# Kernel optimization log

Hardware: AMD Instinct MI355X
Metric: run time of the kernel (lower is better)

## Reference

```python
import jax, jax.numpy as jnp
import numpy as np

B, D, L = 16384, 2048, 6

def setup_inputs() -> dict:
    key = jax.random.key(0)
    kx, kw = jax.random.split(key)
    x = jax.random.normal(kx, (B, D), dtype=jnp.float32)
    # cross weights: xavier_normal on (D,1) -> std = sqrt(2/(D+1)); stacked [L, D]
    std = float(np.sqrt(2.0 / (D + 1)))
    W = jax.random.normal(kw, (L, D), dtype=jnp.float32) * std
    b = jnp.zeros((L, D), dtype=jnp.float32)  # bias params init to zeros
    return {"x": x, "W": W, "b": b}

def reference(x, W, b):
    # Original per layer: x_l = (x0 @ x_l^T) @ w_i + b_i + x_l
    # Algebraically identical: x_l = x0 * (x_l . w_i) + b_i + x_l  (scalar per row)
    x_l = x
    for i in range(W.shape[0]):
        s = jnp.einsum('bd,d->b', x_l, W[i])          # [B]
        x_l = x * s[:, None] + b[i][None, :] + x_l     # [B, D]
    return x_l
```

## Files before the change

kernel.cpp:

```cpp
#include <hip/hip_runtime.h>

#define B_ROWS   16384
#define D_DIM    2048
#define L_LAYERS 6

#define ROW_THREADS 256
#define ROW_WAVES   (ROW_THREADS / 64)
#define ROW_BLOCKS  (B_ROWS / ROW_WAVES)
#define PRE_THREADS 1024
#define WS_FLOATS   (D_DIM + L_LAYERS)

typedef float f32x4 __attribute__((ext_vector_type(4)));


__global__ __launch_bounds__(PRE_THREADS) void precompute_Ue(
    const float* __restrict__ W,
    const float* __restrict__ b,
    float* __restrict__ ws)
{
    __shared__ float red[PRE_THREADS / 64][L_LAYERS];
    const int t    = threadIdx.x;
    const int lane = t & 63;
    const int wid  = t >> 6;
    const int base = t * 2;

    float2 prefix = make_float2(0.f, 0.f);
    float e_red[L_LAYERS];
    #pragma unroll
    for (int l = 0; l < L_LAYERS; ++l) {
        const float2 wv = *(const float2*)(W + l * D_DIM + base);
        const float2 bv = *(const float2*)(b + l * D_DIM + base);
        e_red[l] = prefix.x * wv.x + prefix.y * wv.y;
        prefix.x += bv.x; prefix.y += bv.y;
    }
    *(float2*)(ws + base) = prefix;
    #pragma unroll
    for (int l = 0; l < L_LAYERS; ++l) {
        float v = e_red[l];
        #pragma unroll
        for (int off = 32; off >= 1; off >>= 1) v += __shfl_xor(v, off, 64);
        if (lane == 0) red[wid][l] = v;
    }
    __syncthreads();
    if (t < L_LAYERS) {
        float s = 0.f;
        #pragma unroll
        for (int w = 0; w < PRE_THREADS / 64; ++w) s += red[w][t];
        ws[D_DIM + t] = s;
    }
}

template <bool USE_WS>
__global__ __launch_bounds__(ROW_THREADS) void cross_rows(
    const float* __restrict__ x,
    const float* __restrict__ W,
    const float* __restrict__ b,
    const float* __restrict__ ws,
    float* __restrict__ out)
{
    __shared__ float Ul[D_DIM];
    __shared__ float eLs[L_LAYERS];
    __shared__ float red[ROW_WAVES][L_LAYERS];

    const int t    = threadIdx.x;
    const int lane = t & 63;
    const int wid  = t >> 6;

    if constexpr (USE_WS) {
        const int base = t * 8;
        *(float4*)&Ul[base]     = *(const float4*)(ws + base);
        *(float4*)&Ul[base + 4] = *(const float4*)(ws + base + 4);
        if (t < L_LAYERS) eLs[t] = ws[D_DIM + t];
        __syncthreads();
    } else {
        const int base = t * 8;
        float4 p0 = make_float4(0.f, 0.f, 0.f, 0.f);
        float4 p1 = make_float4(0.f, 0.f, 0.f, 0.f);
        float e_red[L_LAYERS];
        #pragma unroll
        for (int l = 0; l < L_LAYERS; ++l) {
            const float4 w0 = *(const float4*)(W + l * D_DIM + base);
            const float4 w1 = *(const float4*)(W + l * D_DIM + base + 4);
            const float4 b0 = *(const float4*)(b + l * D_DIM + base);
            const float4 b1 = *(const float4*)(b + l * D_DIM + base + 4);
            e_red[l] = p0.x * w0.x + p0.y * w0.y + p0.z * w0.z + p0.w * w0.w
                     + p1.x * w1.x + p1.y * w1.y + p1.z * w1.z + p1.w * w1.w;
            p0.x += b0.x; p0.y += b0.y; p0.z += b0.z; p0.w += b0.w;
            p1.x += b1.x; p1.y += b1.y; p1.z += b1.z; p1.w += b1.w;
        }
        *(float4*)&Ul[base]     = p0;
        *(float4*)&Ul[base + 4] = p1;
        #pragma unroll
        for (int l = 0; l < L_LAYERS; ++l) {
            float v = e_red[l];
            #pragma unroll
            for (int off = 32; off >= 1; off >>= 1) v += __shfl_xor(v, off, 64);
            if (lane == 0) red[wid][l] = v;
        }
        __syncthreads();
        if (t < L_LAYERS) {
            float s = 0.f;
            #pragma unroll
            for (int w = 0; w < ROW_WAVES; ++w) s += red[w][t];
            eLs[t] = s;
        }
        __syncthreads();
    }

    const int gw   = blockIdx.x * ROW_WAVES + wid;
    const float* xr = x + (size_t)gw * D_DIM;
    const int eoff = lane * 4;

    float4 xv[8];
    #pragma unroll
    for (int j = 0; j < 8; ++j) xv[j] = *(const float4*)(xr + j * 256 + eoff);

    float p[L_LAYERS];
    #pragma unroll
    for (int l = 0; l < L_LAYERS; ++l) {
        float a = 0.f;
        #pragma unroll
        for (int j = 0; j < 8; ++j) {
            const float4 wv = *(const float4*)(W + l * D_DIM + j * 256 + eoff);
            a += xv[j].x * wv.x + xv[j].y * wv.y + xv[j].z * wv.z + xv[j].w * wv.w;
        }
        p[l] = a;
    }

    #pragma unroll
    for (int off = 32; off >= 1; off >>= 1) {
        #pragma unroll
        for (int l = 0; l < L_LAYERS; ++l)
            p[l] += __shfl_xor(p[l], off, 64);
    }

    float c = 1.f;
    #pragma unroll
    for (int l = 0; l < L_LAYERS; ++l)
        c = c * (1.f + p[l]) + eLs[l];

    float* orow = out + (size_t)gw * D_DIM;
    #pragma unroll
    for (int j = 0; j < 8; ++j) {
        const float4 uv = *(const float4*)&Ul[j * 256 + eoff];
        f32x4 o;
        o.x = c * xv[j].x + uv.x; o.y = c * xv[j].y + uv.y;
        o.z = c * xv[j].z + uv.z; o.w = c * xv[j].w + uv.w;
        __builtin_nontemporal_store(o, (f32x4*)(orow + j * 256 + eoff));
    }
}

extern "C" void kernel_launch(void* const* d_in, const int* in_sizes, int n_in,
                              void* d_out, int out_size, void* d_ws, size_t ws_size,
                              hipStream_t stream) {
    (void)in_sizes; (void)n_in; (void)out_size;
    const float* x = (const float*)d_in[0];
    const float* W = (const float*)d_in[1];
    const float* b = (const float*)d_in[2];
    float* out = (float*)d_out;

    const bool use_ws = (d_ws != nullptr) && (ws_size >= WS_FLOATS * sizeof(float));
    if (use_ws) {
        float* ws = (float*)d_ws;
        precompute_Ue<<<dim3(1), dim3(PRE_THREADS), 0, stream>>>(W, b, ws);
        cross_rows<true><<<dim3(ROW_BLOCKS), dim3(ROW_THREADS), 0, stream>>>(
            x, W, b, ws, out);
    } else {
        cross_rows<false><<<dim3(ROW_BLOCKS), dim3(ROW_THREADS), 0, stream>>>(
            x, W, b, nullptr, out);
    }
}
```

Before: 251.7 us.

## Process four rows per wave with double-buffered row prefetch

Reduces the grid from one row per wave to four rows per wave (1024 blocks) and software-pipelines the work: the next row's x is loaded into a second register buffer while the current row is reduced and stored. This amortizes the per-block Ul/eL setup and shared-memory fill over more rows and overlaps global loads with compute. In exchange it doubles register use for x, which may lower occupancy, and leaves fewer blocks in flight to hide memory latency.

```diff
diff --git a/kernel.cpp b/kernel.cpp
--- a/kernel.cpp
+++ b/kernel.cpp
@@ -6,9 +6,13 @@
 
 #define ROW_THREADS 256
 #define ROW_WAVES   (ROW_THREADS / 64)
-#define ROW_BLOCKS  (B_ROWS / ROW_WAVES)
+#define ROW_BLOCKS  1024
+#define TOTAL_WAVES (ROW_BLOCKS * ROW_WAVES)
+#define ROWS_PER_WAVE (B_ROWS / TOTAL_WAVES)
 #define PRE_THREADS 1024
 #define WS_FLOATS   (D_DIM + L_LAYERS)
+
+static_assert(ROWS_PER_WAVE == 4, "pipeline below is hand-unrolled for 4");
 
 typedef float f32x4 __attribute__((ext_vector_type(4)));
 
@@ -107,47 +111,59 @@
         __syncthreads();
     }
 
-    const int gw   = blockIdx.x * ROW_WAVES + wid;
-    const float* xr = x + (size_t)gw * D_DIM;
-    const int eoff = lane * 4;
+    const int gw = blockIdx.x * ROW_WAVES + wid;
+    const float* xr = x + (size_t)gw * ROWS_PER_WAVE * D_DIM;
+    float* orow     = out + (size_t)gw * ROWS_PER_WAVE * D_DIM;
+    const int eoff  = lane * 4;
 
-    float4 xv[8];
-    #pragma unroll
-    for (int j = 0; j < 8; ++j) xv[j] = *(const float4*)(xr + j * 256 + eoff);
+    float4 xA[8], xB[8];
 
-    float p[L_LAYERS];
-    #pragma unroll
-    for (int l = 0; l < L_LAYERS; ++l) {
-        float a = 0.f;
+    auto loadRow = [&](float4 (&xv)[8], const float* p) {
+        #pragma unroll
+        for (int j = 0; j < 8; ++j) xv[j] = *(const float4*)(p + j * 256 + eoff);
+    };
+
+    auto computeStore = [&](const float4 (&xv)[8], float* op) {
+        float p[L_LAYERS];
+        #pragma unroll
+        for (int l = 0; l < L_LAYERS; ++l) {
+            float a = 0.f;
+            #pragma unroll
+            for (int j = 0; j < 8; ++j) {
+                const float4 wv = *(const float4*)(W + l * D_DIM + j * 256 + eoff);
+                a += xv[j].x * wv.x + xv[j].y * wv.y
+                   + xv[j].z * wv.z + xv[j].w * wv.w;
+            }
+            p[l] = a;
+        }
+        #pragma unroll
+        for (int off = 32; off >= 1; off >>= 1) {
+            #pragma unroll
+            for (int l = 0; l < L_LAYERS; ++l)
+                p[l] += __shfl_xor(p[l], off, 64);
+        }
+        float c = 1.f;
+        #pragma unroll
+        for (int l = 0; l < L_LAYERS; ++l)
+            c = c * (1.f + p[l]) + eLs[l];
         #pragma unroll
         for (int j = 0; j < 8; ++j) {
-            const float4 wv = *(const float4*)(W + l * D_DIM + j * 256 + eoff);
-            a += xv[j].x * wv.x + xv[j].y * wv.y + xv[j].z * wv.z + xv[j].w * wv.w;
+            const float4 uv = *(const float4*)&Ul[j * 256 + eoff];
+            f32x4 o;
+            o.x = c * xv[j].x + uv.x; o.y = c * xv[j].y + uv.y;
+            o.z = c * xv[j].z + uv.z; o.w = c * xv[j].w + uv.w;
+            __builtin_nontemporal_store(o, (f32x4*)(op + j * 256 + eoff));
         }
-        p[l] = a;
-    }
+    };
 
-    #pragma unroll
-    for (int off = 32; off >= 1; off >>= 1) {
-        #pragma unroll
-        for (int l = 0; l < L_LAYERS; ++l)
-            p[l] += __shfl_xor(p[l], off, 64);
-    }
-
-    float c = 1.f;
-    #pragma unroll
-    for (int l = 0; l < L_LAYERS; ++l)
-        c = c * (1.f + p[l]) + eLs[l];
-
-    float* orow = out + (size_t)gw * D_DIM;
-    #pragma unroll
-    for (int j = 0; j < 8; ++j) {
-        const float4 uv = *(const float4*)&Ul[j * 256 + eoff];
-        f32x4 o;
-        o.x = c * xv[j].x + uv.x; o.y = c * xv[j].y + uv.y;
-        o.z = c * xv[j].z + uv.z; o.w = c * xv[j].w + uv.w;
-        __builtin_nontemporal_store(o, (f32x4*)(orow + j * 256 + eoff));
-    }
+    loadRow(xA, xr);
+    loadRow(xB, xr + D_DIM);
+    computeStore(xA, orow);
+    loadRow(xA, xr + 2 * (size_t)D_DIM);
+    computeStore(xB, orow + D_DIM);
+    loadRow(xB, xr + 3 * (size_t)D_DIM);
+    computeStore(xA, orow + 2 * (size_t)D_DIM);
+    computeStore(xB, orow + 3 * (size_t)D_DIM);
 }
 
 extern "C" void kernel_launch(void* const* d_in, const int* in_sizes, int n_in,
```

New measurement: 307.6 us. 1.22x slower.
